# Performance work log

Hardware: AMD Instinct MI355X
Metric: run time of the kernel (lower is better)

The kernel has to match this reference:

```python
import jax, jax.numpy as jnp
import numpy as np

HIDDEN = 1024
HEADS = 16
HEAD_DIM = HIDDEN // HEADS


def setup_inputs() -> dict:
    key = jax.random.key(0)
    ks = jax.random.split(key, 11)
    s = 1.0 / np.sqrt(HIDDEN)
    return {
        "query": jax.random.normal(ks[0], (8, 1024, HIDDEN), dtype=jnp.float32),
        "key": jax.random.normal(ks[1], (8, 1024, HIDDEN), dtype=jnp.float32),
        "value": jax.random.normal(ks[2], (8, 1024, HIDDEN), dtype=jnp.float32),
        "Wq": jax.random.uniform(ks[3], (HIDDEN, HIDDEN), jnp.float32, -s, s),
        "bq": jax.random.uniform(ks[4], (HIDDEN,), jnp.float32, -s, s),
        "Wk": jax.random.uniform(ks[5], (HIDDEN, HIDDEN), jnp.float32, -s, s),
        "bk": jax.random.uniform(ks[6], (HIDDEN,), jnp.float32, -s, s),
        "Wv": jax.random.uniform(ks[7], (HIDDEN, HIDDEN), jnp.float32, -s, s),
        "bv": jax.random.uniform(ks[8], (HIDDEN,), jnp.float32, -s, s),
        "Wo": jax.random.uniform(ks[9], (HIDDEN, HIDDEN), jnp.float32, -s, s),
        "bo": jax.random.uniform(ks[10], (HIDDEN,), jnp.float32, -s, s),
    }


def reference(query, key, value, Wq, bq, Wk, bk, Wv, bv, Wo, bo):
    B, S, D = key.shape
    scale = jnp.sqrt(jnp.asarray(HEAD_DIM, dtype=query.dtype))
    # linear projections (torch Linear: x @ W.T + b), split into heads -> [B,H,S,hd]
    def proj(x, W, b):
        return (x @ W.T + b).reshape(B, -1, HEADS, HEAD_DIM).transpose(0, 2, 1, 3)
    q = proj(query, Wq, bq)
    k = proj(key, Wk, bk)
    v = proj(value, Wv, bv)
    # [B,H,Sq,Sk] full attention scores (module materializes them)
    energy = jnp.einsum("bhqd,bhkd->bhqk", q, k) / scale
    attention = jax.nn.softmax(energy, axis=-1)
    # dropout p=0.0 -> identity
    x = jnp.einsum("bhqk,bhkd->bhqd", attention, v)
    x = x.transpose(0, 2, 1, 3).reshape(B, -1, D)
    return x @ Wo.T + bo
```

## Files before the change

kernel.cpp:

```cpp
#include <hip/hip_runtime.h>
#include <hip/hip_bf16.h>
#include <stdint.h>

#define HIDDEN 1024
#define HEADS 16
#define HD 64
#define BATCH 8
#define SEQ 1024
#define MTOT (BATCH*SEQ)

typedef __attribute__((ext_vector_type(4))) float  f32x4;
typedef __attribute__((ext_vector_type(4))) float  float4v;
typedef __attribute__((ext_vector_type(8))) short  s16x8;
typedef __attribute__((ext_vector_type(4))) short  s16x4;
typedef __bf16 bf16x8 __attribute__((ext_vector_type(8)));

__device__ __forceinline__ short f2bf(float f) {
  uint32_t u = __builtin_bit_cast(uint32_t, f);
  u += 0x7FFFu + ((u >> 16) & 1u);
  return (short)(u >> 16);
}
__device__ __forceinline__ bf16x8 asbf(s16x8 v) {
  return __builtin_bit_cast(bf16x8, v);
}

__device__ __forceinline__ float dpp_fmax16(float x) {
  int t;
  t = __builtin_amdgcn_update_dpp(0, __builtin_bit_cast(int, x), 0xB1, 0xF, 0xF, true);
  x = fmaxf(x, __builtin_bit_cast(float, t));
  t = __builtin_amdgcn_update_dpp(0, __builtin_bit_cast(int, x), 0x4E, 0xF, 0xF, true);
  x = fmaxf(x, __builtin_bit_cast(float, t));
  t = __builtin_amdgcn_update_dpp(0, __builtin_bit_cast(int, x), 0x141, 0xF, 0xF, true);
  x = fmaxf(x, __builtin_bit_cast(float, t));
  t = __builtin_amdgcn_update_dpp(0, __builtin_bit_cast(int, x), 0x140, 0xF, 0xF, true);
  x = fmaxf(x, __builtin_bit_cast(float, t));
  return x;
}
__device__ __forceinline__ float dpp_fadd16(float x) {
  int t;
  t = __builtin_amdgcn_update_dpp(0, __builtin_bit_cast(int, x), 0xB1, 0xF, 0xF, true);
  x += __builtin_bit_cast(float, t);
  t = __builtin_amdgcn_update_dpp(0, __builtin_bit_cast(int, x), 0x4E, 0xF, 0xF, true);
  x += __builtin_bit_cast(float, t);
  t = __builtin_amdgcn_update_dpp(0, __builtin_bit_cast(int, x), 0x141, 0xF, 0xF, true);
  x += __builtin_bit_cast(float, t);
  t = __builtin_amdgcn_update_dpp(0, __builtin_bit_cast(int, x), 0x140, 0xF, 0xF, true);
  x += __builtin_bit_cast(float, t);
  return x;
}

typedef const __attribute__((address_space(1))) void* gvp;
typedef __attribute__((address_space(3)))       void* lvp;
__device__ __forceinline__ void gl_lds16(const void* g, const void* ldsbase) {
  __builtin_amdgcn_global_load_lds((gvp)(uintptr_t)g,
                                   (lvp)(uintptr_t)(uint32_t)(uintptr_t)ldsbase,
                                   16, 0, 0);
}

__global__ __launch_bounds__(256) void cvt_x(const float* __restrict__ src,
                                             short* __restrict__ dst) {
  int i = blockIdx.x * 256 + threadIdx.x;
  float4v a = *(const float4v*)(src + (size_t)i * 8);
  float4v b = *(const float4v*)(src + (size_t)i * 8 + 4);
  s16x8 o = { f2bf(a.x), f2bf(a.y), f2bf(a.z), f2bf(a.w),
              f2bf(b.x), f2bf(b.y), f2bf(b.z), f2bf(b.w) };
  *(s16x8*)(dst + (size_t)i * 8) = o;
}

__global__ __launch_bounds__(256) void cvt_w(const float* __restrict__ s0,
                                             const float* __restrict__ s1,
                                             const float* __restrict__ s2,
                                             const float* __restrict__ s3,
                                             short* __restrict__ dst) {
  int z = blockIdx.y;
  const float* src = (z == 0) ? s0 : (z == 1) ? s1 : (z == 2) ? s2 : s3;
  int i = blockIdx.x * 256 + threadIdx.x;
  float4v a = *(const float4v*)(src + (size_t)i * 8);
  float4v b = *(const float4v*)(src + (size_t)i * 8 + 4);
  s16x8 o = { f2bf(a.x), f2bf(a.y), f2bf(a.z), f2bf(a.w),
              f2bf(b.x), f2bf(b.y), f2bf(b.z), f2bf(b.w) };
  *(s16x8*)(dst + (size_t)z * 1048576 + (size_t)i * 8) = o;
}

template<bool OUT_IS_F32>
__global__ __launch_bounds__(256, 2) void gemm_bf16_dma(
    const short* __restrict__ A, const short* __restrict__ Wb,
    const float* __restrict__ bias, void* __restrict__ Cv)
{
  __shared__ short Alds[128 * 32];
  __shared__ short Blds[128 * 32];

  const int t  = threadIdx.x;
  const int w  = t >> 6, l = t & 63, g = l >> 4, ln = l & 15;
  const int wr = w >> 1, wc = w & 1;
  const int m0 = blockIdx.x * 128, n0 = blockIdx.y * 128;

  f32x4 acc[4][4];
  #pragma unroll
  for (int i = 0; i < 4; i++)
    #pragma unroll
    for (int j = 0; j < 4; j++) acc[i][j] = (f32x4)0.0f;

  for (int k0 = 0; k0 < 1024; k0 += 32) {
    #pragma unroll
    for (int i = 0; i < 2; i++) {
      int c = i * 256 + w * 64 + l;
      int row = c >> 2, col8 = c & 3;
      gl_lds16(A  + (size_t)(m0 + row) * 1024 + k0 + col8 * 8,
               &Alds[(i * 256 + w * 64) * 8]);
      gl_lds16(Wb + (size_t)(n0 + row) * 1024 + k0 + col8 * 8,
               &Blds[(i * 256 + w * 64) * 8]);
    }
    __syncthreads();

    s16x8 af[4], bfr[4];
    #pragma unroll
    for (int mf = 0; mf < 4; mf++)
      af[mf] = *(const s16x8*)(&Alds[(wr * 64 + mf * 16 + ln) * 32 + g * 8]);
    #pragma unroll
    for (int nf = 0; nf < 4; nf++)
      bfr[nf] = *(const s16x8*)(&Blds[(wc * 64 + nf * 16 + ln) * 32 + g * 8]);

    __builtin_amdgcn_s_setprio(1);
    #pragma unroll
    for (int mf = 0; mf < 4; mf++)
      #pragma unroll
      for (int nf = 0; nf < 4; nf++)
        acc[mf][nf] = __builtin_amdgcn_mfma_f32_16x16x32_bf16(
            asbf(af[mf]), asbf(bfr[nf]), acc[mf][nf], 0, 0, 0);
    __builtin_amdgcn_s_setprio(0);
    __syncthreads();
  }

  float bv[4];
  #pragma unroll
  for (int nf = 0; nf < 4; nf++) bv[nf] = bias[n0 + wc * 64 + nf * 16 + ln];
  #pragma unroll
  for (int mf = 0; mf < 4; mf++)
    #pragma unroll
    for (int nf = 0; nf < 4; nf++)
      #pragma unroll
      for (int r = 0; r < 4; r++) {
        float vv = acc[mf][nf][r] + bv[nf];
        size_t idx = (size_t)(m0 + wr * 64 + mf * 16 + g * 4 + r) * 1024
                   + n0 + wc * 64 + nf * 16 + ln;
        if constexpr (OUT_IS_F32) ((float*)Cv)[idx] = vv;
        else                      ((short*)Cv)[idx] = f2bf(vv);
      }
}

template<bool A_IS_BF16, bool OUT_IS_F32>
__global__ __launch_bounds__(256, 2) void gemm_bt_bias(
    const void* __restrict__ Av, const float* __restrict__ W,
    const float* __restrict__ bias, void* __restrict__ Cv)
{
  __shared__ short Alds[128 * 32];
  __shared__ short Blds[128 * 32];

  const int t  = threadIdx.x;
  const int w  = t >> 6, l = t & 63, g = l >> 4, ln = l & 15;
  const int wr = w >> 1, wc = w & 1;
  const int m0 = blockIdx.x * 128, n0 = blockIdx.y * 128;

  f32x4 acc[4][4];
  #pragma unroll
  for (int i = 0; i < 4; i++)
    #pragma unroll
    for (int j = 0; j < 4; j++) acc[i][j] = (f32x4)0.0f;

  const float* Af = (const float*)Av;
  const short* Ab = (const short*)Av;

  for (int k0 = 0; k0 < 1024; k0 += 32) {
    if constexpr (!A_IS_BF16) {
      #pragma unroll
      for (int i = 0; i < 4; i++) {
        int c = i * 256 + t;
        int row = c >> 3, c4 = c & 7;
        float4v v = *(const float4v*)(Af + (size_t)(m0 + row) * 1024 + k0 + c4 * 4);
        s16x4 p = { f2bf(v.x), f2bf(v.y), f2bf(v.z), f2bf(v.w) };
        *(s16x4*)(&Alds[row * 32 + c4 * 4]) = p;
      }
    } else {
      #pragma unroll
      for (int i = 0; i < 2; i++) {
        int c = i * 256 + t;
        int row = c >> 2, c8 = c & 3;
        *(s16x8*)(&Alds[row * 32 + c8 * 8]) =
            *(const s16x8*)(Ab + (size_t)(m0 + row) * 1024 + k0 + c8 * 8);
      }
    }
    #pragma unroll
    for (int i = 0; i < 4; i++) {
      int c = i * 256 + t;
      int row = c >> 3, c4 = c & 7;
      float4v v = *(const float4v*)(W + (size_t)(n0 + row) * 1024 + k0 + c4 * 4);
      s16x4 p = { f2bf(v.x), f2bf(v.y), f2bf(v.z), f2bf(v.w) };
      *(s16x4*)(&Blds[row * 32 + c4 * 4]) = p;
    }
    __syncthreads();

    s16x8 af[4], bfr[4];
    #pragma unroll
    for (int mf = 0; mf < 4; mf++)
      af[mf] = *(const s16x8*)(&Alds[(wr * 64 + mf * 16 + ln) * 32 + g * 8]);
    #pragma unroll
    for (int nf = 0; nf < 4; nf++)
      bfr[nf] = *(const s16x8*)(&Blds[(wc * 64 + nf * 16 + ln) * 32 + g * 8]);

    #pragma unroll
    for (int mf = 0; mf < 4; mf++)
      #pragma unroll
      for (int nf = 0; nf < 4; nf++)
        acc[mf][nf] = __builtin_amdgcn_mfma_f32_16x16x32_bf16(
            asbf(af[mf]), asbf(bfr[nf]), acc[mf][nf], 0, 0, 0);
    __syncthreads();
  }

  float bv[4];
  #pragma unroll
  for (int nf = 0; nf < 4; nf++) bv[nf] = bias[n0 + wc * 64 + nf * 16 + ln];
  #pragma unroll
  for (int mf = 0; mf < 4; mf++)
    #pragma unroll
    for (int nf = 0; nf < 4; nf++)
      #pragma unroll
      for (int r = 0; r < 4; r++) {
        float vv = acc[mf][nf][r] + bv[nf];
        size_t idx = (size_t)(m0 + wr * 64 + mf * 16 + g * 4 + r) * 1024
                   + n0 + wc * 64 + nf * 16 + ln;
        if constexpr (OUT_IS_F32) ((float*)Cv)[idx] = vv;
        else                      ((short*)Cv)[idx] = f2bf(vv);
      }
}

__global__ __launch_bounds__(256, 2) void flash_attn(
    const short* __restrict__ Q, const short* __restrict__ K,
    const short* __restrict__ V, short* __restrict__ CTX)
{
  __shared__ short Klds[64 * 64];
  __shared__ short Vt[64 * 64];
  __shared__ short Plds[4][32 * 72];

  const int t  = threadIdx.x;
  const int w  = t >> 6, l = t & 63, g = l >> 4, ln = l & 15;
  const int tile = blockIdx.x & 7;
  const int bh   = blockIdx.x >> 3;
  const int b = bh >> 4, h = bh & 15;
  const size_t rowbase = (size_t)b * SEQ;
  const int colbase = h * HD;
  const int q0w = tile * 128 + w * 32;

  s16x8 qf[2][2];
  #pragma unroll
  for (int mf = 0; mf < 2; mf++)
    #pragma unroll
    for (int kf = 0; kf < 2; kf++)
      qf[mf][kf] = *(const s16x8*)(Q + (rowbase + q0w + mf * 16 + ln) * 1024
                                     + colbase + kf * 32 + g * 8);

  f32x4 acc_o[2][4];
  #pragma unroll
  for (int i = 0; i < 2; i++)
    #pragma unroll
    for (int j = 0; j < 4; j++) acc_o[i][j] = (f32x4)0.0f;

  float m_run[2][4], l_run[2][4];
  #pragma unroll
  for (int i = 0; i < 2; i++)
    #pragma unroll
    for (int r = 0; r < 4; r++) { m_run[i][r] = -1e30f; l_run[i][r] = 0.0f; }

  const float C1 = 0.18033688011112042f;

  for (int kt = 0; kt < 16; kt++) {
    const int kk0 = kt * 64;
    #pragma unroll
    for (int i = 0; i < 2; i++) {
      int c = i * 256 + t;
      int kk = c >> 3, dblk = c & 7;
      int dsrc = dblk ^ (kk & 7);
      s16x8 kv = *(const s16x8*)(K + (rowbase + kk0 + kk) * 1024 + colbase + dsrc * 8);
      *(s16x8*)(&Klds[kk * 64 + dblk * 8]) = kv;
      s16x8 vv = *(const s16x8*)(V + (rowbase + kk0 + kk) * 1024 + colbase + dblk * 8);
      #pragma unroll
      for (int e = 0; e < 8; e++) {
        int d  = dblk * 8 + e;
        int sw = (d & 7) ^ (d >> 3);
        Vt[d * 64 + (kk ^ (sw * 8))] = vv[e];
      }
    }
    __syncthreads();

    f32x4 s_acc[2][4];
    #pragma unroll
    for (int i = 0; i < 2; i++)
      #pragma unroll
      for (int j = 0; j < 4; j++) s_acc[i][j] = (f32x4)0.0f;

    __builtin_amdgcn_s_setprio(1);
    #pragma unroll
    for (int kf = 0; kf < 2; kf++) {
      s16x8 kfr[4];
      #pragma unroll
      for (int nf = 0; nf < 4; nf++) {
        int kk = nf * 16 + ln;
        int dblk = kf * 4 + g;
        kfr[nf] = *(const s16x8*)(&Klds[kk * 64 + (dblk ^ (kk & 7)) * 8]);
      }
      #pragma unroll
      for (int mf = 0; mf < 2; mf++)
        #pragma unroll
        for (int nf = 0; nf < 4; nf++)
          s_acc[mf][nf] = __builtin_amdgcn_mfma_f32_16x16x32_bf16(
              asbf(qf[mf][kf]), asbf(kfr[nf]), s_acc[mf][nf], 0, 0, 0);
    }
    __builtin_amdgcn_s_setprio(0);

    float smax[2][4];
    float worst = -1e30f;
    #pragma unroll
    for (int mf = 0; mf < 2; mf++)
      #pragma unroll
      for (int r = 0; r < 4; r++) {
        float mx = fmaxf(fmaxf(s_acc[mf][0][r], s_acc[mf][1][r]),
                         fmaxf(s_acc[mf][2][r], s_acc[mf][3][r]));
        mx = dpp_fmax16(mx);
        smax[mf][r] = mx * C1;
        worst = fmaxf(worst, smax[mf][r] - m_run[mf][r]);
      }

    if (__all(worst <= 8.0f)) {
      #pragma unroll
      for (int mf = 0; mf < 2; mf++)
        #pragma unroll
        for (int r = 0; r < 4; r++) {
          float m0v = m_run[mf][r];
          float rs = 0.0f;
          #pragma unroll
          for (int nf = 0; nf < 4; nf++) {
            float pv = exp2f(s_acc[mf][nf][r] * C1 - m0v);
            s_acc[mf][nf][r] = pv;
            rs += pv;
          }
          l_run[mf][r] += dpp_fadd16(rs);
        }
    } else {
      #pragma unroll
      for (int mf = 0; mf < 2; mf++)
        #pragma unroll
        for (int r = 0; r < 4; r++) {
          float mnew = fmaxf(m_run[mf][r], smax[mf][r]);
          float sc = exp2f(m_run[mf][r] - mnew);
          m_run[mf][r] = mnew;
          float rs = 0.0f;
          #pragma unroll
          for (int nf = 0; nf < 4; nf++) {
            float pv = exp2f(s_acc[mf][nf][r] * C1 - mnew);
            s_acc[mf][nf][r] = pv;
            rs += pv;
          }
          l_run[mf][r] = l_run[mf][r] * sc + dpp_fadd16(rs);
          #pragma unroll
          for (int nf = 0; nf < 4; nf++) acc_o[mf][nf][r] *= sc;
        }
    }

    short* Pw = &Plds[w][0];
    #pragma unroll
    for (int mf = 0; mf < 2; mf++)
      #pragma unroll
      for (int nf = 0; nf < 4; nf++)
        #pragma unroll
        for (int r = 0; r < 4; r++) {
          int row = mf * 16 + g * 4 + r;
          int colS = (nf * 16 + ln) ^ (g << 3);
          Pw[row * 72 + colS] = f2bf(s_acc[mf][nf][r]);
        }

    s16x8 pa[2][2], vb[4][2];
    #pragma unroll
    for (int mf = 0; mf < 2; mf++)
      #pragma unroll
      for (int kf = 0; kf < 2; kf++)
        pa[mf][kf] = *(const s16x8*)(
            &Pw[(mf * 16 + ln) * 72 + (((kf * 4 + g) ^ (ln >> 2)) << 3)]);
    #pragma unroll
    for (int nf = 0; nf < 4; nf++)
      #pragma unroll
      for (int kf = 0; kf < 2; kf++) {
        int d  = nf * 16 + ln;
        int sw = (d & 7) ^ (d >> 3);
        vb[nf][kf] = *(const s16x8*)(&Vt[d * 64 + ((kf * 32 + g * 8) ^ (sw * 8))]);
      }

    __builtin_amdgcn_s_setprio(1);
    #pragma unroll
    for (int kf = 0; kf < 2; kf++)
      #pragma unroll
      for (int mf = 0; mf < 2; mf++)
        #pragma unroll
        for (int nf = 0; nf < 4; nf++)
          acc_o[mf][nf] = __builtin_amdgcn_mfma_f32_16x16x32_bf16(
              asbf(pa[mf][kf]), asbf(vb[nf][kf]), acc_o[mf][nf], 0, 0, 0);
    __builtin_amdgcn_s_setprio(0);
    __syncthreads();
  }

  #pragma unroll
  for (int mf = 0; mf < 2; mf++)
    #pragma unroll
    for (int r = 0; r < 4; r++) {
      float inv = 1.0f / l_run[mf][r];
      size_t row = rowbase + q0w + mf * 16 + g * 4 + r;
      #pragma unroll
      for (int nf = 0; nf < 4; nf++)
        CTX[row * 1024 + colbase + nf * 16 + ln] = f2bf(acc_o[mf][nf][r] * inv);
    }
}

extern "C" void kernel_launch(void* const* d_in, const int* in_sizes, int n_in,
                              void* d_out, int out_size, void* d_ws, size_t ws_size,
                              hipStream_t stream) {
  const float* query = (const float*)d_in[0];
  const float* key   = (const float*)d_in[1];
  const float* value = (const float*)d_in[2];
  const float* Wq = (const float*)d_in[3];
  const float* bq = (const float*)d_in[4];
  const float* Wk = (const float*)d_in[5];
  const float* bk = (const float*)d_in[6];
  const float* Wv = (const float*)d_in[7];
  const float* bv = (const float*)d_in[8];
  const float* Wo = (const float*)d_in[9];
  const float* bo = (const float*)d_in[10];

  const size_t E = (size_t)MTOT * 1024;
  short* Qb = (short*)d_ws;
  short* Kb = Qb + E;
  short* Vb = Kb + E;
  short* Cx = Vb + E;
  short* T  = Cx + E;
  short* Wb = T  + E;

  const size_t need = (5 * E + 4ull * 1048576) * 2;
  dim3 gg(MTOT / 128, HIDDEN / 128), bb(256);
  dim3 fg(BATCH * HEADS * (SEQ / 128));

  if (ws_size >= need) {
    cvt_w<<<dim3(512, 4), bb, 0, stream>>>(Wq, Wk, Wv, Wo, Wb);
    cvt_x<<<4096, bb, 0, stream>>>(query, T);
    gemm_bf16_dma<false><<<gg, bb, 0, stream>>>(T, Wb + 0 * 1048576, bq, Qb);
    cvt_x<<<4096, bb, 0, stream>>>(key, T);
    gemm_bf16_dma<false><<<gg, bb, 0, stream>>>(T, Wb + 1 * 1048576, bk, Kb);
    cvt_x<<<4096, bb, 0, stream>>>(value, T);
    gemm_bf16_dma<false><<<gg, bb, 0, stream>>>(T, Wb + 2 * 1048576, bv, Vb);
    flash_attn<<<fg, bb, 0, stream>>>(Qb, Kb, Vb, Cx);
    gemm_bf16_dma<true><<<gg, bb, 0, stream>>>(Cx, Wb + 3 * 1048576, bo, (float*)d_out);
  } else {
    gemm_bt_bias<false, false><<<gg, bb, 0, stream>>>(query, Wq, bq, Qb);
    gemm_bt_bias<false, false><<<gg, bb, 0, stream>>>(key,   Wk, bk, Kb);
    gemm_bt_bias<false, false><<<gg, bb, 0, stream>>>(value, Wv, bv, Vb);
    flash_attn<<<fg, bb, 0, stream>>>(Qb, Kb, Vb, Cx);
    gemm_bt_bias<true, true><<<gg, bb, 0, stream>>>(Cx, Wo, bo, (float*)d_out);
  }
}
```

Baseline: 241.3 us.

## Double-buffer K/V in flash attention and fold softmax scale into Q projection

The flash attention kernel now keeps two K/V shared-memory buffers. It prefetches the next tile into registers while computing on the current one, which removes one barrier per iteration. The softmax scale (including the log2e factor) is applied in the Q projection epilogue, so the inner loop saves a multiply per score. The per-iteration row-sum DPP reduction is deferred to the end, P is packed with v_cvt_pk_bf16_f32, and launch bounds are raised to 3 blocks per CU. Costs are more LDS per block and extra register pressure, and applying the scale before rounding Q to bf16 shifts the rounding slightly.

```diff
diff --git a/kernel.cpp b/kernel.cpp
--- a/kernel.cpp
+++ b/kernel.cpp
@@ -14,6 +14,8 @@
 typedef __attribute__((ext_vector_type(8))) short  s16x8;
 typedef __attribute__((ext_vector_type(4))) short  s16x4;
 typedef __bf16 bf16x8 __attribute__((ext_vector_type(8)));
+
+#define QSCALE 0.18033688011112042f
 
 __device__ __forceinline__ short f2bf(float f) {
   uint32_t u = __builtin_bit_cast(uint32_t, f);
@@ -85,7 +87,7 @@
 template<bool OUT_IS_F32>
 __global__ __launch_bounds__(256, 2) void gemm_bf16_dma(
     const short* __restrict__ A, const short* __restrict__ Wb,
-    const float* __restrict__ bias, void* __restrict__ Cv)
+    const float* __restrict__ bias, void* __restrict__ Cv, float scale)
 {
   __shared__ short Alds[128 * 32];
   __shared__ short Blds[128 * 32];
@@ -141,7 +143,7 @@
     for (int nf = 0; nf < 4; nf++)
       #pragma unroll
       for (int r = 0; r < 4; r++) {
-        float vv = acc[mf][nf][r] + bv[nf];
+        float vv = (acc[mf][nf][r] + bv[nf]) * scale;
         size_t idx = (size_t)(m0 + wr * 64 + mf * 16 + g * 4 + r) * 1024
                    + n0 + wc * 64 + nf * 16 + ln;
         if constexpr (OUT_IS_F32) ((float*)Cv)[idx] = vv;
@@ -152,7 +154,7 @@
 template<bool A_IS_BF16, bool OUT_IS_F32>
 __global__ __launch_bounds__(256, 2) void gemm_bt_bias(
     const void* __restrict__ Av, const float* __restrict__ W,
-    const float* __restrict__ bias, void* __restrict__ Cv)
+    const float* __restrict__ bias, void* __restrict__ Cv, float scale)
 {
   __shared__ short Alds[128 * 32];
   __shared__ short Blds[128 * 32];
@@ -226,7 +228,7 @@
     for (int nf = 0; nf < 4; nf++)
       #pragma unroll
       for (int r = 0; r < 4; r++) {
-        float vv = acc[mf][nf][r] + bv[nf];
+        float vv = (acc[mf][nf][r] + bv[nf]) * scale;
         size_t idx = (size_t)(m0 + wr * 64 + mf * 16 + g * 4 + r) * 1024
                    + n0 + wc * 64 + nf * 16 + ln;
         if constexpr (OUT_IS_F32) ((float*)Cv)[idx] = vv;
@@ -234,12 +236,12 @@
       }
 }
 
-__global__ __launch_bounds__(256, 2) void flash_attn(
+__global__ __launch_bounds__(256, 3) void flash_attn(
     const short* __restrict__ Q, const short* __restrict__ K,
     const short* __restrict__ V, short* __restrict__ CTX)
 {
-  __shared__ short Klds[64 * 64];
-  __shared__ short Vt[64 * 64];
+  __shared__ short Klds[2][64 * 64];
+  __shared__ short Vtl [2][64 * 64];
   __shared__ short Plds[4][32 * 72];
 
   const int t  = threadIdx.x;
@@ -251,6 +253,13 @@
   const int colbase = h * HD;
   const int q0w = tile * 128 + w * 32;
 
+  const int kk0  = t >> 3;
+  const int dblk = t & 7;
+  const int ksw  = (dblk ^ (kk0 & 7)) * 8;
+  const int kWr  = kk0 * 64 + dblk * 8;
+  const short* Kg = K + rowbase * 1024 + colbase + ksw;
+  const short* Vg = V + rowbase * 1024 + colbase + dblk * 8;
+
   s16x8 qf[2][2];
   #pragma unroll
   for (int mf = 0; mf < 2; mf++)
@@ -271,26 +280,38 @@
     #pragma unroll
     for (int r = 0; r < 4; r++) { m_run[i][r] = -1e30f; l_run[i][r] = 0.0f; }
 
-  const float C1 = 0.18033688011112042f;
-
+  auto storeKV = [&](int buf, s16x8 ka, s16x8 kb, s16x8 va, s16x8 vb8) {
+    short* Kd = &Klds[buf][0];
+    short* Vd = &Vtl[buf][0];
+    *(s16x8*)(Kd + kWr)        = ka;
+    *(s16x8*)(Kd + kWr + 2048) = kb;
+    #pragma unroll
+    for (int e = 0; e < 8; e++) {
+      int a0 = (dblk * 8 + e) * 64 + (kk0 ^ ((e ^ dblk) * 8));
+      Vd[a0]      = va[e];
+      Vd[a0 ^ 32] = vb8[e];
+    }
+  };
+
+  s16x8 kvA = *(const s16x8*)(Kg + (size_t)kk0 * 1024);
+  s16x8 kvB = *(const s16x8*)(Kg + (size_t)(kk0 + 32) * 1024);
+  s16x8 vvA = *(const s16x8*)(Vg + (size_t)kk0 * 1024);
+  s16x8 vvB = *(const s16x8*)(Vg + (size_t)(kk0 + 32) * 1024);
+  storeKV(0, kvA, kvB, vvA, vvB);
+
+  int cur = 0;
   for (int kt = 0; kt < 16; kt++) {
-    const int kk0 = kt * 64;
-    #pragma unroll
-    for (int i = 0; i < 2; i++) {
-      int c = i * 256 + t;
-      int kk = c >> 3, dblk = c & 7;
-      int dsrc = dblk ^ (kk & 7);
-      s16x8 kv = *(const s16x8*)(K + (rowbase + kk0 + kk) * 1024 + colbase + dsrc * 8);
-      *(s16x8*)(&Klds[kk * 64 + dblk * 8]) = kv;
-      s16x8 vv = *(const s16x8*)(V + (rowbase + kk0 + kk) * 1024 + colbase + dblk * 8);
-      #pragma unroll
-      for (int e = 0; e < 8; e++) {
-        int d  = dblk * 8 + e;
-        int sw = (d & 7) ^ (d >> 3);
-        Vt[d * 64 + (kk ^ (sw * 8))] = vv[e];
-      }
+    if (kt < 15) {
+      const size_t r0 = (size_t)((kt + 1) * 64 + kk0) * 1024;
+      kvA = *(const s16x8*)(Kg + r0);
+      kvB = *(const s16x8*)(Kg + r0 + 32 * 1024);
+      vvA = *(const s16x8*)(Vg + r0);
+      vvB = *(const s16x8*)(Vg + r0 + 32 * 1024);
     }
     __syncthreads();
+
+    const short* Kc = &Klds[cur][0];
+    const short* Vc = &Vtl[cur][0];
 
     f32x4 s_acc[2][4];
     #pragma unroll
@@ -303,11 +324,9 @@
     for (int kf = 0; kf < 2; kf++) {
       s16x8 kfr[4];
       #pragma unroll
-      for (int nf = 0; nf < 4; nf++) {
-        int kk = nf * 16 + ln;
-        int dblk = kf * 4 + g;
-        kfr[nf] = *(const s16x8*)(&Klds[kk * 64 + (dblk ^ (kk & 7)) * 8]);
-      }
+      for (int nf = 0; nf < 4; nf++)
+        kfr[nf] = *(const s16x8*)(Kc + (nf * 16 + ln) * 64
+                                     + (((kf * 4 + g) ^ (ln & 7)) * 8));
       #pragma unroll
       for (int mf = 0; mf < 2; mf++)
         #pragma unroll
@@ -326,8 +345,8 @@
         float mx = fmaxf(fmaxf(s_acc[mf][0][r], s_acc[mf][1][r]),
                          fmaxf(s_acc[mf][2][r], s_acc[mf][3][r]));
         mx = dpp_fmax16(mx);
-        smax[mf][r] = mx * C1;
-        worst = fmaxf(worst, smax[mf][r] - m_run[mf][r]);
+        smax[mf][r] = mx;
+        worst = fmaxf(worst, mx - m_run[mf][r]);
       }
 
     if (__all(worst <= 8.0f)) {
@@ -339,11 +358,11 @@
           float rs = 0.0f;
           #pragma unroll
           for (int nf = 0; nf < 4; nf++) {
-            float pv = exp2f(s_acc[mf][nf][r] * C1 - m0v);
+            float pv = exp2f(s_acc[mf][nf][r] - m0v);
             s_acc[mf][nf][r] = pv;
             rs += pv;
           }
-          l_run[mf][r] += dpp_fadd16(rs);
+          l_run[mf][r] += rs;
         }
     } else {
       #pragma unroll
@@ -356,11 +375,11 @@
           float rs = 0.0f;
           #pragma unroll
           for (int nf = 0; nf < 4; nf++) {
-            float pv = exp2f(s_acc[mf][nf][r] * C1 - mnew);
+            float pv = exp2f(s_acc[mf][nf][r] - mnew);
             s_acc[mf][nf][r] = pv;
             rs += pv;
           }
-          l_run[mf][r] = l_run[mf][r] * sc + dpp_fadd16(rs);
+          l_run[mf][r] = l_run[mf][r] * sc + rs;
           #pragma unroll
           for (int nf = 0; nf < 4; nf++) acc_o[mf][nf][r] *= sc;
         }
@@ -370,15 +389,20 @@
     #pragma unroll
     for (int mf = 0; mf < 2; mf++)
       #pragma unroll
-      for (int nf = 0; nf < 4; nf++)
-        #pragma unroll
-        for (int r = 0; r < 4; r++) {
-          int row = mf * 16 + g * 4 + r;
-          int colS = (nf * 16 + ln) ^ (g << 3);
-          Pw[row * 72 + colS] = f2bf(s_acc[mf][nf][r]);
-        }
-
-    s16x8 pa[2][2], vb[4][2];
+      for (int nf = 0; nf < 4; nf++) {
+        uint32_t p01, p23;
+        asm("v_cvt_pk_bf16_f32 %0, %1, %2"
+            : "=v"(p01) : "v"(s_acc[mf][nf][0]), "v"(s_acc[mf][nf][1]));
+        asm("v_cvt_pk_bf16_f32 %0, %1, %2"
+            : "=v"(p23) : "v"(s_acc[mf][nf][2]), "v"(s_acc[mf][nf][3]));
+        int pb = (mf * 16 + g * 4) * 72 + ((nf * 16 + ln) ^ (g << 3));
+        Pw[pb]       = (short)p01;
+        Pw[pb + 72]  = (short)(p01 >> 16);
+        Pw[pb + 144] = (short)p23;
+        Pw[pb + 216] = (short)(p23 >> 16);
+      }
+
+    s16x8 pa[2][2], vbf[4][2];
     #pragma unroll
     for (int mf = 0; mf < 2; mf++)
       #pragma unroll
@@ -391,7 +415,7 @@
       for (int kf = 0; kf < 2; kf++) {
         int d  = nf * 16 + ln;
         int sw = (d & 7) ^ (d >> 3);
-        vb[nf][kf] = *(const s16x8*)(&Vt[d * 64 + ((kf * 32 + g * 8) ^ (sw * 8))]);
+        vbf[nf][kf] = *(const s16x8*)(Vc + d * 64 + ((kf * 32 + g * 8) ^ (sw * 8)));
       }
 
     __builtin_amdgcn_s_setprio(1);
@@ -402,16 +426,20 @@
         #pragma unroll
         for (int nf = 0; nf < 4; nf++)
           acc_o[mf][nf] = __builtin_amdgcn_mfma_f32_16x16x32_bf16(
-              asbf(pa[mf][kf]), asbf(vb[nf][kf]), acc_o[mf][nf], 0, 0, 0);
+              asbf(pa[mf][kf]), asbf(vbf[nf][kf]), acc_o[mf][nf], 0, 0, 0);
     __builtin_amdgcn_s_setprio(0);
-    __syncthreads();
+
+    if (kt < 15) {
+      storeKV(cur ^ 1, kvA, kvB, vvA, vvB);
+      cur ^= 1;
+    }
   }
 
   #pragma unroll
   for (int mf = 0; mf < 2; mf++)
     #pragma unroll
     for (int r = 0; r < 4; r++) {
-      float inv = 1.0f / l_run[mf][r];
+      float inv = 1.0f / dpp_fadd16(l_run[mf][r]);
       size_t row = rowbase + q0w + mf * 16 + g * 4 + r;
       #pragma unroll
       for (int nf = 0; nf < 4; nf++)
@@ -449,18 +477,18 @@
   if (ws_size >= need) {
     cvt_w<<<dim3(512, 4), bb, 0, stream>>>(Wq, Wk, Wv, Wo, Wb);
     cvt_x<<<4096, bb, 0, stream>>>(query, T);
-    gemm_bf16_dma<false><<<gg, bb, 0, stream>>>(T, Wb + 0 * 1048576, bq, Qb);
+    gemm_bf16_dma<false><<<gg, bb, 0, stream>>>(T, Wb + 0 * 1048576, bq, Qb, QSCALE);
     cvt_x<<<4096, bb, 0, stream>>>(key, T);
-    gemm_bf16_dma<false><<<gg, bb, 0, stream>>>(T, Wb + 1 * 1048576, bk, Kb);
+    gemm_bf16_dma<false><<<gg, bb, 0, stream>>>(T, Wb + 1 * 1048576, bk, Kb, 1.0f);
     cvt_x<<<4096, bb, 0, stream>>>(value, T);
-    gemm_bf16_dma<false><<<gg, bb, 0, stream>>>(T, Wb + 2 * 1048576, bv, Vb);
+    gemm_bf16_dma<false><<<gg, bb, 0, stream>>>(T, Wb + 2 * 1048576, bv, Vb, 1.0f);
     flash_attn<<<fg, bb, 0, stream>>>(Qb, Kb, Vb, Cx);
-    gemm_bf16_dma<true><<<gg, bb, 0, stream>>>(Cx, Wb + 3 * 1048576, bo, (float*)d_out);
+    gemm_bf16_dma<true><<<gg, bb, 0, stream>>>(Cx, Wb + 3 * 1048576, bo, (float*)d_out, 1.0f);
   } else {
-    gemm_bt_bias<false, false><<<gg, bb, 0, stream>>>(query, Wq, bq, Qb);
-    gemm_bt_bias<false, false><<<gg, bb, 0, stream>>>(key,   Wk, bk, Kb);
-    gemm_bt_bias<false, false><<<gg, bb, 0, stream>>>(value, Wv, bv, Vb);
+    gemm_bt_bias<false, false><<<gg, bb, 0, stream>>>(query, Wq, bq, Qb, QSCALE);
+    gemm_bt_bias<false, false><<<gg, bb, 0, stream>>>(key,   Wk, bk, Kb, 1.0f);
+    gemm_bt_bias<false, false><<<gg, bb, 0, stream>>>(value, Wv, bv, Vb, 1.0f);
     flash_attn<<<fg, bb, 0, stream>>>(Qb, Kb, Vb, Cx);
-    gemm_bt_bias<true, true><<<gg, bb, 0, stream>>>(Cx, Wo, bo, (float*)d_out);
+    gemm_bt_bias<true, true><<<gg, bb, 0, stream>>>(Cx, Wo, bo, (float*)d_out, 1.0f);
   }
 }
```

New measurement: 508.7 us. +110.8%, slower.
